# Optimization experiments

Measured on AMD Instinct MI355X. Metric: run time of the kernel, lower is better.

The kernel has to match this reference:

```python
import jax, jax.numpy as jnp
import numpy as np
import math

B, T, D, H, FFN_DIM, SE_HID = 16, 1024, 512, 8, 2048, 256
EPS = 1e-5  # torch LayerNorm default


def layer_norm(x, g, b):
    mu = jnp.mean(x, axis=-1, keepdims=True)
    var = jnp.mean((x - mu) ** 2, axis=-1, keepdims=True)
    return (x - mu) * jax.lax.rsqrt(var + EPS) * g + b


def setup_inputs() -> dict:
    key = jax.random.key(0)
    ks = jax.random.split(key, 8)
    s = 0.02
    return {
        "x": jax.random.normal(ks[0], (B, T, D), dtype=jnp.float32),
        "wq": jax.random.normal(ks[1], (D, D), dtype=jnp.float32) * s,
        "wk": jax.random.normal(ks[2], (D, D), dtype=jnp.float32) * s,
        "wv": jax.random.normal(ks[3], (D, D), dtype=jnp.float32) * s,
        "ln1_g": jnp.ones((D,), jnp.float32),
        "ln1_b": jnp.zeros((D,), jnp.float32),
        "se_w1": jax.random.normal(ks[4], (T, SE_HID), dtype=jnp.float32) * s,
        "se_w2": jax.random.normal(ks[5], (SE_HID, T), dtype=jnp.float32) * s,
        "ffn_g": jnp.ones((D,), jnp.float32),
        "ffn_b": jnp.zeros((D,), jnp.float32),
        "w1": jax.random.normal(ks[6], (D, FFN_DIM), dtype=jnp.float32) * s,
        "b1": jnp.zeros((FFN_DIM,), jnp.float32),
        "w2": jax.random.normal(ks[7], (FFN_DIM, D), dtype=jnp.float32) * s,
        "b2": jnp.zeros((D,), jnp.float32),
    }


def _forward(x, wq, wk, wv, ln1_g, ln1_b, se_w1, se_w2, ffn_g, ffn_b, w1, b1, w2, b2):
    # --- SE gate over the sequence axis: squeeze over feature dim D ---
    y = jnp.mean(x, axis=-1)                       # (B, T)
    gate = jax.nn.sigmoid(jax.nn.relu(y @ se_w1) @ se_w2)  # (B, T)
    x = x + x * gate[..., None]

    d = D // H
    n = layer_norm(x, ln1_g, ln1_b)
    q = (n @ wq).reshape(B, T, H, d)
    k = (n @ wk).reshape(B, T, H, d)
    v = (n @ wv).reshape(B, T, H, d)
    attn = jnp.einsum('bnhd,bmhd->bnmh', q, k) / math.sqrt(d)
    w = jax.nn.softmax(attn, axis=2)               # softmax over key dim m
    x = x + jnp.einsum('bnmh,bmhd->bnhd', w, v).reshape(B, T, D)

    # --- FFN (pre-norm, exact GELU as nn.GELU default) ---
    n2 = layer_norm(x, ffn_g, ffn_b)
    h = jax.nn.gelu(n2 @ w1 + b1, approximate=False)
    return x + (h @ w2 + b2)


def reference(x, wq, wk, wv, ln1_g, ln1_b, se_w1, se_w2, ffn_g, ffn_b, w1, b1, w2, b2):
    return _forward(x, wq, wk, wv, ln1_g, ln1_b, se_w1, se_w2, ffn_g, ffn_b, w1, b1, w2, b2)
```

## Files before the change

kernel.cpp:

```cpp
#include <hip/hip_runtime.h>

typedef unsigned int uint32;

using bf16x8 = __attribute__((ext_vector_type(8))) short;
using f32x4  = __attribute__((ext_vector_type(4))) float;

#define B_  16
#define T_  1024
#define D_  512
#define H_  8
#define HD_ 64
#define FFN_ 2048
#define SEH_ 256
#define EPS_ 1e-5f

#define AS1 __attribute__((address_space(1)))
#define AS3 __attribute__((address_space(3)))

__device__ __forceinline__ ushort f2bf(float f) {
  uint32 x = __float_as_uint(f);
  return (ushort)((x + 0x7fffu + ((x >> 16) & 1u)) >> 16);
}
__device__ __forceinline__ float bf2f(ushort u) {
  return __uint_as_float(((uint32)u) << 16);
}
__device__ __forceinline__ float gelu_fast(float v) {
  float u = v * (0.7978845608f + 0.0356774081f * v * v);
  float e = __expf(2.0f * u);
  float t = 1.0f - 2.0f * __builtin_amdgcn_rcpf(e + 1.0f);
  return 0.5f * v * (1.0f + t);
}

__global__ __launch_bounds__(256) void cast_transpose_all_k(
    const float* __restrict__ wq, const float* __restrict__ wk,
    const float* __restrict__ wv, const float* __restrict__ w1,
    const float* __restrict__ w2, ushort* __restrict__ wqkvT,
    ushort* __restrict__ w1T, ushort* __restrict__ w2T) {
  __shared__ float tile[32][33];
  int bid = blockIdx.x;
  const float* W; ushort* WT; int K, N, bk, bn;
  if (bid < 768) {
    int w = bid >> 8, r = bid & 255;
    W = (w == 0) ? wq : (w == 1) ? wk : wv;
    WT = wqkvT + (size_t)w * 512 * 512;
    K = 512; N = 512; bk = (r >> 4) * 32; bn = (r & 15) * 32;
  } else if (bid < 1792) {
    int r = bid - 768;
    W = w1; WT = w1T; K = 512; N = 2048; bk = (r >> 6) * 32; bn = (r & 63) * 32;
  } else {
    int r = bid - 1792;
    W = w2; WT = w2T; K = 2048; N = 512; bk = (r >> 4) * 32; bn = (r & 15) * 32;
  }
  int lx = threadIdx.x & 31;
  int ly = threadIdx.x >> 5;
  #pragma unroll
  for (int i = ly; i < 32; i += 8)
    tile[i][lx] = W[(size_t)(bk + i) * N + bn + lx];
  __syncthreads();
  #pragma unroll
  for (int i = ly; i < 32; i += 8)
    WT[(size_t)(bn + i) * K + bk + lx] = f2bf(tile[lx][i]);
}

__global__ __launch_bounds__(256) void se_rowmean_k(const float* __restrict__ x,
                                                    float* __restrict__ y) {
  int row  = blockIdx.x * 4 + (threadIdx.x >> 6);
  int lane = threadIdx.x & 63;
  const float4* p = (const float4*)(x + (size_t)row * D_);
  float4 a = p[lane * 2];
  float4 b = p[lane * 2 + 1];
  float s = a.x + a.y + a.z + a.w + b.x + b.y + b.z + b.w;
  #pragma unroll
  for (int m = 1; m < 64; m <<= 1) s += __shfl_xor(s, m);
  if (lane == 0) y[row] = s * (1.0f / D_);
}

__global__ __launch_bounds__(256) void se_mlp1_k(const float* __restrict__ y,
                                                 const float* __restrict__ w1,
                                                 float* __restrict__ z) {
  __shared__ float yb[T_];
  __shared__ float part[8][32];
  int b = blockIdx.x, jt = blockIdx.y;
  int tid = threadIdx.x;
  #pragma unroll
  for (int i = 0; i < 4; i++) yb[tid + i * 256] = y[(size_t)b * T_ + tid + i * 256];
  __syncthreads();
  int tj = tid & 31, tk = tid >> 5;
  int j = jt * 32 + tj;
  const float* wp = w1 + (size_t)(tk * 128) * SEH_ + j;
  const float* yp = yb + tk * 128;
  float a0 = 0.f, a1 = 0.f, a2 = 0.f, a3 = 0.f;
  #pragma unroll
  for (int t = 0; t < 128; t += 4) {
    a0 += yp[t]     * wp[(t)     * SEH_];
    a1 += yp[t + 1] * wp[(t + 1) * SEH_];
    a2 += yp[t + 2] * wp[(t + 2) * SEH_];
    a3 += yp[t + 3] * wp[(t + 3) * SEH_];
  }
  part[tk][tj] = (a0 + a1) + (a2 + a3);
  __syncthreads();
  if (tid < 32) {
    float s = 0.f;
    #pragma unroll
    for (int k = 0; k < 8; k++) s += part[k][tid];
    z[(size_t)b * SEH_ + jt * 32 + tid] = fmaxf(s, 0.f);
  }
}

__global__ __launch_bounds__(256) void se_mlp2_k(const float* __restrict__ z,
                                                 const float* __restrict__ w2,
                                                 float* __restrict__ gate) {
  __shared__ float zb[SEH_];
  __shared__ float part[2][128];
  int b = blockIdx.x, bt = blockIdx.y;
  int tid = threadIdx.x;
  zb[tid & 255] = z[(size_t)b * SEH_ + (tid & 255)];
  __syncthreads();
  int tt = tid & 127, tk = tid >> 7;
  int t = bt * 128 + tt;
  const float* wp = w2 + (size_t)(tk * 128) * T_ + t;
  const float* zp = zb + tk * 128;
  float a0 = 0.f, a1 = 0.f, a2 = 0.f, a3 = 0.f;
  #pragma unroll
  for (int j = 0; j < 128; j += 4) {
    a0 += zp[j]     * wp[(j)     * T_];
    a1 += zp[j + 1] * wp[(j + 1) * T_];
    a2 += zp[j + 2] * wp[(j + 2) * T_];
    a3 += zp[j + 3] * wp[(j + 3) * T_];
  }
  part[tk][tt] = (a0 + a1) + (a2 + a3);
  __syncthreads();
  if (tid < 128) {
    float s = part[0][tid] + part[1][tid];
    gate[(size_t)b * T_ + bt * 128 + tid] = 1.0f / (1.0f + __expf(-s));
  }
}

__global__ __launch_bounds__(256) void gate_ln1_k(
    const float* __restrict__ x, const float* __restrict__ gate,
    const float* __restrict__ g, const float* __restrict__ beta,
    float* __restrict__ x1, ushort* __restrict__ nbuf) {
  int rid  = blockIdx.x * 4 + (threadIdx.x >> 6);
  int lane = threadIdx.x & 63;
  const float4* xr = (const float4*)(x + (size_t)rid * D_);
  float4 a = xr[lane * 2];
  float4 b = xr[lane * 2 + 1];
  float gv = 1.0f + gate[rid];
  a.x *= gv; a.y *= gv; a.z *= gv; a.w *= gv;
  b.x *= gv; b.y *= gv; b.z *= gv; b.w *= gv;
  float4* x1r = (float4*)(x1 + (size_t)rid * D_);
  x1r[lane * 2]     = a;
  x1r[lane * 2 + 1] = b;
  float s  = a.x + a.y + a.z + a.w + b.x + b.y + b.z + b.w;
  float ss = a.x*a.x + a.y*a.y + a.z*a.z + a.w*a.w + b.x*b.x + b.y*b.y + b.z*b.z + b.w*b.w;
  #pragma unroll
  for (int m = 1; m < 64; m <<= 1) { s += __shfl_xor(s, m); ss += __shfl_xor(ss, m); }
  float mu   = s * (1.0f / D_);
  float var  = ss * (1.0f / D_) - mu * mu;
  float rstd = rsqrtf(var + EPS_);
  const float4* gp = (const float4*)g;
  const float4* bp = (const float4*)beta;
  float4 g0 = gp[lane * 2], g1 = gp[lane * 2 + 1];
  float4 b0 = bp[lane * 2], b1 = bp[lane * 2 + 1];
  union { uint4 v; ushort u[8]; } pk;
  pk.u[0] = f2bf((a.x - mu) * rstd * g0.x + b0.x);
  pk.u[1] = f2bf((a.y - mu) * rstd * g0.y + b0.y);
  pk.u[2] = f2bf((a.z - mu) * rstd * g0.z + b0.z);
  pk.u[3] = f2bf((a.w - mu) * rstd * g0.w + b0.w);
  pk.u[4] = f2bf((b.x - mu) * rstd * g1.x + b1.x);
  pk.u[5] = f2bf((b.y - mu) * rstd * g1.y + b1.y);
  pk.u[6] = f2bf((b.z - mu) * rstd * g1.z + b1.z);
  pk.u[7] = f2bf((b.w - mu) * rstd * g1.w + b1.w);
  *(uint4*)(nbuf + (size_t)rid * D_ + lane * 8) = pk.v;
}

__global__ __launch_bounds__(256) void ln2_k(
    const float* __restrict__ x2, const float* __restrict__ g,
    const float* __restrict__ beta, ushort* __restrict__ nbuf) {
  int rid  = blockIdx.x * 4 + (threadIdx.x >> 6);
  int lane = threadIdx.x & 63;
  const float4* xr = (const float4*)(x2 + (size_t)rid * D_);
  float4 a = xr[lane * 2];
  float4 b = xr[lane * 2 + 1];
  float s  = a.x + a.y + a.z + a.w + b.x + b.y + b.z + b.w;
  float ss = a.x*a.x + a.y*a.y + a.z*a.z + a.w*a.w + b.x*b.x + b.y*b.y + b.z*b.z + b.w*b.w;
  #pragma unroll
  for (int m = 1; m < 64; m <<= 1) { s += __shfl_xor(s, m); ss += __shfl_xor(ss, m); }
  float mu   = s * (1.0f / D_);
  float var  = ss * (1.0f / D_) - mu * mu;
  float rstd = rsqrtf(var + EPS_);
  const float4* gp = (const float4*)g;
  const float4* bp = (const float4*)beta;
  float4 g0 = gp[lane * 2], g1 = gp[lane * 2 + 1];
  float4 b0 = bp[lane * 2], b1 = bp[lane * 2 + 1];
  union { uint4 v; ushort u[8]; } pk;
  pk.u[0] = f2bf((a.x - mu) * rstd * g0.x + b0.x);
  pk.u[1] = f2bf((a.y - mu) * rstd * g0.y + b0.y);
  pk.u[2] = f2bf((a.z - mu) * rstd * g0.z + b0.z);
  pk.u[3] = f2bf((a.w - mu) * rstd * g0.w + b0.w);
  pk.u[4] = f2bf((b.x - mu) * rstd * g1.x + b1.x);
  pk.u[5] = f2bf((b.y - mu) * rstd * g1.y + b1.y);
  pk.u[6] = f2bf((b.z - mu) * rstd * g1.z + b1.z);
  pk.u[7] = f2bf((b.w - mu) * rstd * g1.w + b1.w);
  *(uint4*)(nbuf + (size_t)rid * D_ + lane * 8) = pk.v;
}

#define MFMA16 __builtin_amdgcn_mfma_f32_16x16x32_bf16
template <int BN>
__global__ __launch_bounds__(512, 2) void gemm256_k(
    const ushort* __restrict__ A, const ushort* __restrict__ BT,
    int M, int N, int K,
    const float* __restrict__ bias, const float* __restrict__ resid,
    ushort* __restrict__ outB, ushort* __restrict__ outB2,
    ushort* __restrict__ vTout, float* __restrict__ outF, int epi) {
  constexpr int WNS   = BN / 4;
  constexpr int NT    = BN / 64;
  constexpr int NH    = NT / 2;
  constexpr int BROWS = BN / 8;
  constexpr int BJ    = BN / 64;
  __shared__ ushort smem[2 * 256 * 64 + 2 * BN * 64];
  ushort* As = smem;
  ushort* Bs = smem + 2 * 256 * 64;

  int tid  = threadIdx.x;
  int wave = tid >> 6;
  int lane = tid & 63;
  int quad = lane >> 4;
  int l15  = lane & 15;
  int wm   = wave >> 2;
  int wn   = wave & 3;
  int lr   = lane >> 3;
  int lcs  = (lane & 7) ^ lr;

  int nbk = N / BN;
  int bid = blockIdx.x;
  int xcd = bid & 7;
  int sb  = bid >> 3;
  int n0  = (sb % nbk) * BN;
  int m0  = ((sb / nbk) * 8 + xcd) * 256;

  f32x4 acc[8][NT];
  #pragma unroll
  for (int i = 0; i < 8; i++)
    #pragma unroll
    for (int j = 0; j < NT; j++) acc[i][j] = (f32x4){0.f, 0.f, 0.f, 0.f};

  const ushort* Ag = A  + (size_t)(m0 + wave * 32 + lr) * K + lcs * 8;
  const ushort* Bg = BT + (size_t)(n0 + wave * BROWS + lr) * K + lcs * 8;

  auto STAGE = [&](int t, int buf) {
    int ko = t * 64;
    ushort* da = As + buf * (256 * 64) + wave * (32 * 64);
    #pragma unroll
    for (int j = 0; j < 4; j++)
      __builtin_amdgcn_global_load_lds((const AS1 void*)(Ag + ko + (size_t)(j * 8) * K),
                                       (AS3 void*)(da + j * 512), 16, 0, 0);
    ushort* db = Bs + buf * (BN * 64) + wave * (BROWS * 64);
    #pragma unroll
    for (int j = 0; j < BJ; j++)
      __builtin_amdgcn_global_load_lds((const AS1 void*)(Bg + ko + (size_t)(j * 8) * K),
                                       (AS3 void*)(db + j * 512), 16, 0, 0);
  };

  int ntt = K >> 6;
  STAGE(0, 0);
  STAGE(1, 1);
  if constexpr (BN == 256) asm volatile("s_waitcnt vmcnt(8)" ::: "memory");
  else                     asm volatile("s_waitcnt vmcnt(6)" ::: "memory");
  __builtin_amdgcn_s_barrier();

  const ushort* Arow = As + (wm * 128 + l15) * 64;
  const ushort* Brow = Bs + (wn * WNS + l15) * 64;
  int c0 = ((0 + quad) ^ (l15 & 7)) * 8;
  int c1 = ((4 + quad) ^ (l15 & 7)) * 8;

  for (int t = 0; t < ntt; ++t) {
    const ushort* Ab = Arow + (t & 1) * (256 * 64);
    const ushort* Bb = Brow + (t & 1) * (BN * 64);
    bf16x8 a[4][2], b[NT][2];

    #pragma unroll
    for (int m4 = 0; m4 < 4; m4++) {
      a[m4][0] = *(const bf16x8*)(Ab + m4 * 1024 + c0);
      a[m4][1] = *(const bf16x8*)(Ab + m4 * 1024 + c1);
    }
    #pragma unroll
    for (int h = 0; h < NH; h++) {
      b[h][0] = *(const bf16x8*)(Bb + h * 1024 + c0);
      b[h][1] = *(const bf16x8*)(Bb + h * 1024 + c1);
    }
    __builtin_amdgcn_s_barrier();
    asm volatile("s_waitcnt lgkmcnt(0)" ::: "memory");
    __builtin_amdgcn_sched_barrier(0);
    __builtin_amdgcn_s_setprio(1);
    #pragma unroll
    for (int m4 = 0; m4 < 4; m4++)
      #pragma unroll
      for (int h = 0; h < NH; h++) {
        acc[m4][h] = MFMA16(a[m4][0], b[h][0], acc[m4][h], 0, 0, 0);
        acc[m4][h] = MFMA16(a[m4][1], b[h][1], acc[m4][h], 0, 0, 0);
      }
    __builtin_amdgcn_s_setprio(0);
    __builtin_amdgcn_s_barrier();

    #pragma unroll
    for (int h = 0; h < NH; h++) {
      b[NH + h][0] = *(const bf16x8*)(Bb + (NH + h) * 1024 + c0);
      b[NH + h][1] = *(const bf16x8*)(Bb + (NH + h) * 1024 + c1);
    }
    __builtin_amdgcn_s_barrier();
    asm volatile("s_waitcnt lgkmcnt(0)" ::: "memory");
    __builtin_amdgcn_sched_barrier(0);
    __builtin_amdgcn_s_setprio(1);
    #pragma unroll
    for (int m4 = 0; m4 < 4; m4++)
      #pragma unroll
      for (int h = 0; h < NH; h++) {
        acc[m4][NH + h] = MFMA16(a[m4][0], b[NH + h][0], acc[m4][NH + h], 0, 0, 0);
        acc[m4][NH + h] = MFMA16(a[m4][1], b[NH + h][1], acc[m4][NH + h], 0, 0, 0);
      }
    __builtin_amdgcn_s_setprio(0);
    __builtin_amdgcn_s_barrier();

    #pragma unroll
    for (int m4 = 0; m4 < 4; m4++) {
      a[m4][0] = *(const bf16x8*)(Ab + (4 + m4) * 1024 + c0);
      a[m4][1] = *(const bf16x8*)(Ab + (4 + m4) * 1024 + c1);
    }
    __builtin_amdgcn_s_barrier();
    asm volatile("s_waitcnt lgkmcnt(0)" ::: "memory");
    __builtin_amdgcn_sched_barrier(0);
    __builtin_amdgcn_s_setprio(1);
    #pragma unroll
    for (int m4 = 0; m4 < 4; m4++)
      #pragma unroll
      for (int h = 0; h < NH; h++) {
        acc[4 + m4][h] = MFMA16(a[m4][0], b[h][0], acc[4 + m4][h], 0, 0, 0);
        acc[4 + m4][h] = MFMA16(a[m4][1], b[h][1], acc[4 + m4][h], 0, 0, 0);
      }
    __builtin_amdgcn_s_setprio(0);
    __builtin_amdgcn_s_barrier();

    __builtin_amdgcn_s_setprio(1);
    #pragma unroll
    for (int m4 = 0; m4 < 4; m4++)
      #pragma unroll
      for (int h = 0; h < NH; h++) {
        acc[4 + m4][NH + h] = MFMA16(a[m4][0], b[NH + h][0], acc[4 + m4][NH + h], 0, 0, 0);
        acc[4 + m4][NH + h] = MFMA16(a[m4][1], b[NH + h][1], acc[4 + m4][NH + h], 0, 0, 0);
      }
    __builtin_amdgcn_s_setprio(0);

    if (t + 1 < ntt) {
      if (t + 2 < ntt) {
        STAGE(t + 2, t & 1);
        if constexpr (BN == 256) asm volatile("s_waitcnt vmcnt(8)" ::: "memory");
        else                     asm volatile("s_waitcnt vmcnt(6)" ::: "memory");
      } else {
        asm volatile("s_waitcnt vmcnt(0)" ::: "memory");
      }
      __builtin_amdgcn_s_barrier();
    }
  }

  int colbase = n0 + wn * WNS;
  if (epi == 2) {
    #pragma unroll
    for (int nt = 0; nt < NT; nt++) {
      int n = colbase + nt * 16 + l15;
      float bv = bias[n];
      #pragma unroll
      for (int mt = 0; mt < 8; mt++) {
        int m = m0 + wm * 128 + mt * 16 + quad * 4;
        #pragma unroll
        for (int r = 0; r < 4; r++) {
          size_t idx = (size_t)(m + r) * N + n;
          outF[idx] = acc[mt][nt][r] + bv + resid[idx];
        }
      }
    }
  } else {
    __syncthreads();
    if (epi == 3 && n0 >= 1024) {
      constexpr int TST = 136;
      ushort* tb = smem + wave * (32 * TST);
      #pragma unroll
      for (int nt = 0; nt < NT; nt++) {
        int dloc = nt * 16 + l15;
        #pragma unroll
        for (int mt = 0; mt < 8; mt++) {
          ushort4 pk;
          pk.x = f2bf(acc[mt][nt][0]);
          pk.y = f2bf(acc[mt][nt][1]);
          pk.z = f2bf(acc[mt][nt][2]);
          pk.w = f2bf(acc[mt][nt][3]);
          *(ushort4*)(tb + dloc * TST + mt * 16 + quad * 4) = pk;
        }
      }
      int dbase = (n0 - 1024) + wn * WNS;
      int bb = m0 >> 10;
      int tg = (m0 & 1023) + wm * 128 + l15 * 8;
      #pragma unroll
      for (int j = 0; j < 8; j++) {
        int dloc = j * 4 + quad;
        int d = dbase + dloc;
        int hh = d >> 6, dd = d & 63;
        uint4 vv = *(const uint4*)(tb + dloc * TST + l15 * 8);
        *(uint4*)(vTout + (((size_t)bb * 8 + hh) * 64 + dd) * 1024 + tg) = vv;
      }
    } else {
      constexpr int RS  = WNS + 8;
      constexpr int LPR = WNS / 8;
      constexpr int RPS = 64 / LPR;
      ushort* tb = smem + wave * (32 * RS);
      ushort* gout; int ldN; float scl;
      if (epi == 1) { gout = outB; ldN = N; scl = 1.0f; }
      else {
        gout = (n0 < 512) ? outB : outB2; ldN = 512;
        scl = (n0 < 512) ? 0.18033688011112042f : 1.0f;
      }
      int ncol = (epi == 1) ? colbase : ((n0 & 511) + wn * WNS);
      float bv[NT];
      #pragma unroll
      for (int nt = 0; nt < NT; nt++)
        bv[nt] = (epi == 1) ? bias[colbase + nt * 16 + l15] : 0.0f;
      int rrow = lane / LPR;
      int seg  = lane % LPR;
      int mrow0 = m0 + wm * 128;
      #pragma unroll
      for (int mtg = 0; mtg < 4; mtg++) {
        #pragma unroll
        for (int mh = 0; mh < 2; mh++) {
          int mt = mtg * 2 + mh;
          #pragma unroll
          for (int nt = 0; nt < NT; nt++) {
            #pragma unroll
            for (int r = 0; r < 4; r++) {
              float v = (epi == 1) ? gelu_fast(acc[mt][nt][r] + bv[nt])
                                   : acc[mt][nt][r] * scl;
              tb[(mh * 16 + quad * 4 + r) * RS + nt * 16 + l15] = f2bf(v);
            }
          }
        }
        #pragma unroll
        for (int it = 0; it < 32 / RPS; it++) {
          int rl = it * RPS + rrow;
          uint4 v = *(const uint4*)(tb + rl * RS + seg * 8);
          *(uint4*)(gout + (size_t)(mrow0 + mtg * 32 + rl) * ldN + ncol + seg * 8) = v;
        }
      }
    }
  }
}

__global__ __launch_bounds__(256) void attn_k(
    const ushort* __restrict__ q, const ushort* __restrict__ k,
    const ushort* __restrict__ vT, const float* __restrict__ x1,
    float* __restrict__ out) {
  __shared__ ushort Ks[64 * 64];
  __shared__ ushort Vs[64 * 64];
  __shared__ ushort Ps[128 * 64];
  int bid = blockIdx.x;
  int xcd = bid & 7;
  int j   = bid >> 3;
  int qt  = j & 7;
  int pair = xcd * 16 + (j >> 3);
  int b = pair >> 3;
  int h = pair & 7;
  int t0 = qt * 128;
  int tid  = threadIdx.x;
  int wave = tid >> 6;
  int lane = tid & 63;
  int quad = lane >> 4;
  int l15  = lane & 15;

  const ushort* qp0 = q + ((size_t)(b * T_ + t0 + wave * 16 + l15)) * D_ + h * HD_;
  const ushort* qp1 = qp0 + (size_t)64 * D_;
  bf16x8 aq0 = *(const bf16x8*)(qp0 + quad * 8);
  bf16x8 aq1 = *(const bf16x8*)(qp0 + 32 + quad * 8);
  bf16x8 aq2 = *(const bf16x8*)(qp1 + quad * 8);
  bf16x8 aq3 = *(const bf16x8*)(qp1 + 32 + quad * 8);

  int srow = tid >> 2;
  int c2   = (tid & 3) * 2;
  int scol = c2 * 8;
  int sw0  = ((c2)     ^ (srow & 7)) << 3;
  int sw1  = ((c2 + 1) ^ (srow & 7)) << 3;
  int swb  = srow * 64;
  int rsw0 = ((quad)     ^ (l15 & 7)) << 3;
  int rsw1 = ((quad + 4) ^ (l15 & 7)) << 3;

  float l_part[2][4] = {{0.f, 0.f, 0.f, 0.f}, {0.f, 0.f, 0.f, 0.f}};
  f32x4 o0[4], o1[4];
  #pragma unroll
  for (int dt = 0; dt < 4; dt++) {
    o0[dt] = (f32x4){0.f, 0.f, 0.f, 0.f};
    o1[dt] = (f32x4){0.f, 0.f, 0.f, 0.f};
  }

  const ushort* vTb = vT + ((size_t)(b * 8 + h) * 64 + srow) * 1024 + scol;
  size_t kgb = ((size_t)(b * T_ + srow)) * D_ + h * HD_ + scol;

  uint4 ku0 = *(const uint4*)(k + kgb);
  uint4 ku1 = *(const uint4*)(k + kgb + 8);
  uint4 vv0 = *(const uint4*)(vTb);
  uint4 vv1 = *(const uint4*)(vTb + 8);

  for (int kt = 0; kt < 16; kt++) {
    __syncthreads();

    *(uint4*)(Ks + swb + sw0) = ku0;
    *(uint4*)(Ks + swb + sw1) = ku1;
    *(uint4*)(Vs + swb + sw0) = vv0;
    *(uint4*)(Vs + swb + sw1) = vv1;

    __syncthreads();

    if (kt + 1 < 16) {
      size_t kg2 = kgb + (size_t)(kt + 1) * 64 * D_;
      const ushort* vp2 = vTb + (kt + 1) * 64;
      ku0 = *(const uint4*)(k + kg2);
      ku1 = *(const uint4*)(k + kg2 + 8);
      vv0 = *(const uint4*)(vp2);
      vv1 = *(const uint4*)(vp2 + 8);
    }

    f32x4 s0[4], s1[4];
    #pragma unroll
    for (int nt = 0; nt < 4; nt++) {
      const ushort* krow = Ks + (nt * 16 + l15) * 64;
      bf16x8 bk0 = *(const bf16x8*)(krow + rsw0);
      bf16x8 bk1 = *(const bf16x8*)(krow + rsw1);
      f32x4 z = (f32x4){0.f, 0.f, 0.f, 0.f};
      s0[nt] = MFMA16(aq0, bk0, z, 0, 0, 0);
      s0[nt] = MFMA16(aq1, bk1, s0[nt], 0, 0, 0);
      s1[nt] = MFMA16(aq2, bk0, z, 0, 0, 0);
      s1[nt] = MFMA16(aq3, bk1, s1[nt], 0, 0, 0);
    }

    #pragma unroll
    for (int nt = 0; nt < 4; nt++) {
      int cps = nt * 2 + (l15 >> 3);
      #pragma unroll
      for (int r = 0; r < 4; r++) {
        int rowl = quad * 4 + r;
        int off = (wave * 16 + rowl) * 64 + ((cps ^ (rowl & 7)) << 3) + (l15 & 7);
        float p0 = __builtin_amdgcn_exp2f(s0[nt][r]);
        float p1 = __builtin_amdgcn_exp2f(s1[nt][r]);
        l_part[0][r] += p0;
        l_part[1][r] += p1;
        Ps[off]            = f2bf(p0);
        Ps[off + 64 * 64]  = f2bf(p1);
      }
    }

    const ushort* prow = Ps + (wave * 16 + l15) * 64;
    bf16x8 ap0 = *(const bf16x8*)(prow + rsw0);
    bf16x8 ap1 = *(const bf16x8*)(prow + rsw1);
    bf16x8 ap2 = *(const bf16x8*)(prow + 4096 + rsw0);
    bf16x8 ap3 = *(const bf16x8*)(prow + 4096 + rsw1);
    #pragma unroll
    for (int dt = 0; dt < 4; dt++) {
      const ushort* vrow = Vs + (dt * 16 + l15) * 64;
      bf16x8 bv0 = *(const bf16x8*)(vrow + rsw0);
      bf16x8 bv1 = *(const bf16x8*)(vrow + rsw1);
      o0[dt] = MFMA16(ap0, bv0, o0[dt], 0, 0, 0);
      o0[dt] = MFMA16(ap1, bv1, o0[dt], 0, 0, 0);
      o1[dt] = MFMA16(ap2, bv0, o1[dt], 0, 0, 0);
      o1[dt] = MFMA16(ap3, bv1, o1[dt], 0, 0, 0);
    }
  }

  #pragma unroll
  for (int s = 0; s < 2; s++) {
    f32x4* oo = s ? o1 : o0;
    #pragma unroll
    for (int r = 0; r < 4; r++) {
      float l = l_part[s][r];
      l += __shfl_xor(l, 1);
      l += __shfl_xor(l, 2);
      l += __shfl_xor(l, 4);
      l += __shfl_xor(l, 8);
      float inv = 1.0f / l;
      int qrow = t0 + s * 64 + wave * 16 + quad * 4 + r;
      size_t base = ((size_t)(b * T_ + qrow)) * D_ + h * HD_;
      #pragma unroll
      for (int dt = 0; dt < 4; dt++) {
        size_t idx = base + dt * 16 + l15;
        out[idx] = x1[idx] + oo[dt][r] * inv;
      }
    }
  }
}

extern "C" void kernel_launch(void* const* d_in, const int* in_sizes, int n_in,
                              void* d_out, int out_size, void* d_ws, size_t ws_size,
                              hipStream_t stream) {
  (void)in_sizes; (void)n_in; (void)out_size; (void)ws_size;
  const float* x     = (const float*)d_in[0];
  const float* wq    = (const float*)d_in[1];
  const float* wk    = (const float*)d_in[2];
  const float* wv    = (const float*)d_in[3];
  const float* ln1_g = (const float*)d_in[4];
  const float* ln1_b = (const float*)d_in[5];
  const float* se_w1 = (const float*)d_in[6];
  const float* se_w2 = (const float*)d_in[7];
  const float* ffn_g = (const float*)d_in[8];
  const float* ffn_b = (const float*)d_in[9];
  const float* w1    = (const float*)d_in[10];
  const float* b1    = (const float*)d_in[11];
  const float* w2    = (const float*)d_in[12];
  const float* b2    = (const float*)d_in[13];
  float* out = (float*)d_out;
  char* ws = (char*)d_ws;

  constexpr size_t X1_OFF   = 0;
  constexpr size_t N_OFF    = 33554432;
  constexpr size_t Q_OFF    = 50331648;
  constexpr size_t K_OFF    = 67108864;
  constexpr size_t V_OFF    = 83886080;
  constexpr size_t H_OFF    = 50331648;
  constexpr size_t WQKV_OFF = 117440512;
  constexpr size_t W1T_OFF  = 119013376;
  constexpr size_t W2T_OFF  = 121110528;
  constexpr size_t Y_OFF    = 123207680;
  constexpr size_t Z_OFF    = 123273216;
  constexpr size_t GATE_OFF = 123289600;

  float*  x1    = (float*)(ws + X1_OFF);
  ushort* nbuf  = (ushort*)(ws + N_OFF);
  ushort* qb    = (ushort*)(ws + Q_OFF);
  ushort* kb    = (ushort*)(ws + K_OFF);
  ushort* vT    = (ushort*)(ws + V_OFF);
  ushort* hb    = (ushort*)(ws + H_OFF);
  ushort* wqkvT = (ushort*)(ws + WQKV_OFF);
  ushort* w1T   = (ushort*)(ws + W1T_OFF);
  ushort* w2T   = (ushort*)(ws + W2T_OFF);
  float*  yv    = (float*)(ws + Y_OFF);
  float*  zv    = (float*)(ws + Z_OFF);
  float*  gate  = (float*)(ws + GATE_OFF);

  const int M = B_ * T_;

  cast_transpose_all_k<<<2816, 256, 0, stream>>>(wq, wk, wv, w1, w2, wqkvT, w1T, w2T);

  se_rowmean_k<<<M / 4, 256, 0, stream>>>(x, yv);
  se_mlp1_k<<<dim3(B_, 8), 256, 0, stream>>>(yv, se_w1, zv);
  se_mlp2_k<<<dim3(B_, 8), 256, 0, stream>>>(zv, se_w2, gate);

  gate_ln1_k<<<M / 4, 256, 0, stream>>>(x, gate, ln1_g, ln1_b, x1, nbuf);

  gemm256_k<128><<<(M / 256) * (1536 / 128), 512, 0, stream>>>(
      nbuf, wqkvT, M, 1536, D_, nullptr, nullptr, qb, kb, vT, nullptr, 3);

  attn_k<<<B_ * H_ * (T_ / 128), 256, 0, stream>>>(qb, kb, vT, x1, out);

  ln2_k<<<M / 4, 256, 0, stream>>>(out, ffn_g, ffn_b, nbuf);

  gemm256_k<256><<<(M / 256) * (FFN_ / 256), 512, 0, stream>>>(
      nbuf, w1T, M, FFN_, D_, b1, nullptr, hb, nullptr, nullptr, nullptr, 1);
  gemm256_k<128><<<(M / 256) * (D_ / 128), 512, 0, stream>>>(
      hb, w2T, M, D_, FFN_, b2, out, nullptr, nullptr, nullptr, out, 2);
}
```

Baseline: 344.7 us.

## Double-buffer attention K/V via direct global-to-LDS loads with larger query tiles

The attention kernel now handles 256 query rows per block with 512 threads, halving how often each K/V tile is loaded per query. K/V tiles are staged straight into double-buffered LDS with global_load_lds, so the register round trip is gone and the next tile's load overlaps compute. Each iteration needs one barrier instead of two. The softmax exp is fused into the QK loop and uses a packed bf16 convert. This uses more LDS per block and launches half as many blocks, which may lower occupancy and raise tail effects.

```diff
diff --git a/kernel.cpp b/kernel.cpp
--- a/kernel.cpp
+++ b/kernel.cpp
@@ -23,6 +23,11 @@
 }
 __device__ __forceinline__ float bf2f(ushort u) {
   return __uint_as_float(((uint32)u) << 16);
+}
+__device__ __forceinline__ uint32 cvtpk(float a, float b) {
+  uint32 r;
+  asm("v_cvt_pk_bf16_f32 %0, %1, %2" : "=v"(r) : "v"(a), "v"(b));
+  return r;
 }
 __device__ __forceinline__ float gelu_fast(float v) {
   float u = v * (0.7978845608f + 0.0356774081f * v * v);
@@ -453,40 +458,50 @@
   }
 }
 
-__global__ __launch_bounds__(256) void attn_k(
+__global__ __launch_bounds__(512, 2) void attn_k(
     const ushort* __restrict__ q, const ushort* __restrict__ k,
     const ushort* __restrict__ vT, const float* __restrict__ x1,
     float* __restrict__ out) {
-  __shared__ ushort Ks[64 * 64];
-  __shared__ ushort Vs[64 * 64];
-  __shared__ ushort Ps[128 * 64];
+  __shared__ ushort Ks[2 * 64 * 64];
+  __shared__ ushort Vs[2 * 64 * 64];
+  __shared__ ushort Ps[256 * 64];
   int bid = blockIdx.x;
   int xcd = bid & 7;
   int j   = bid >> 3;
-  int qt  = j & 7;
-  int pair = xcd * 16 + (j >> 3);
+  int qt  = j & 3;
+  int pair = xcd * 16 + (j >> 2);
   int b = pair >> 3;
   int h = pair & 7;
-  int t0 = qt * 128;
+  int t0 = qt * 256;
   int tid  = threadIdx.x;
   int wave = tid >> 6;
   int lane = tid & 63;
   int quad = lane >> 4;
   int l15  = lane & 15;
 
+  int row8 = lane >> 3;
+  int csw  = ((lane & 7) ^ row8) * 8;
+  const ushort* kst = k + ((size_t)(b * T_ + wave * 8 + row8)) * D_ + h * HD_ + csw;
+  const ushort* vst = vT + ((size_t)((b * 8 + h) * 64 + wave * 8 + row8)) * 1024 + csw;
+  ushort* KsW = Ks + wave * 512;
+  ushort* VsW = Vs + wave * 512;
+
+  auto STAGE = [&](int kt, int buf) {
+    __builtin_amdgcn_global_load_lds((const AS1 void*)(kst + (size_t)kt * 64 * D_),
+                                     (AS3 void*)(KsW + buf * 4096), 16, 0, 0);
+    __builtin_amdgcn_global_load_lds((const AS1 void*)(vst + kt * 64),
+                                     (AS3 void*)(VsW + buf * 4096), 16, 0, 0);
+  };
+
+  STAGE(0, 0);
+
   const ushort* qp0 = q + ((size_t)(b * T_ + t0 + wave * 16 + l15)) * D_ + h * HD_;
-  const ushort* qp1 = qp0 + (size_t)64 * D_;
+  const ushort* qp1 = qp0 + (size_t)128 * D_;
   bf16x8 aq0 = *(const bf16x8*)(qp0 + quad * 8);
   bf16x8 aq1 = *(const bf16x8*)(qp0 + 32 + quad * 8);
   bf16x8 aq2 = *(const bf16x8*)(qp1 + quad * 8);
   bf16x8 aq3 = *(const bf16x8*)(qp1 + 32 + quad * 8);
 
-  int srow = tid >> 2;
-  int c2   = (tid & 3) * 2;
-  int scol = c2 * 8;
-  int sw0  = ((c2)     ^ (srow & 7)) << 3;
-  int sw1  = ((c2 + 1) ^ (srow & 7)) << 3;
-  int swb  = srow * 64;
   int rsw0 = ((quad)     ^ (l15 & 7)) << 3;
   int rsw1 = ((quad + 4) ^ (l15 & 7)) << 3;
 
@@ -498,70 +513,58 @@
     o1[dt] = (f32x4){0.f, 0.f, 0.f, 0.f};
   }
 
-  const ushort* vTb = vT + ((size_t)(b * 8 + h) * 64 + srow) * 1024 + scol;
-  size_t kgb = ((size_t)(b * T_ + srow)) * D_ + h * HD_ + scol;
-
-  uint4 ku0 = *(const uint4*)(k + kgb);
-  uint4 ku1 = *(const uint4*)(k + kgb + 8);
-  uint4 vv0 = *(const uint4*)(vTb);
-  uint4 vv1 = *(const uint4*)(vTb + 8);
+  asm volatile("s_waitcnt vmcnt(0)" ::: "memory");
+  __syncthreads();
 
   for (int kt = 0; kt < 16; kt++) {
-    __syncthreads();
-
-    *(uint4*)(Ks + swb + sw0) = ku0;
-    *(uint4*)(Ks + swb + sw1) = ku1;
-    *(uint4*)(Vs + swb + sw0) = vv0;
-    *(uint4*)(Vs + swb + sw1) = vv1;
-
-    __syncthreads();
-
-    if (kt + 1 < 16) {
-      size_t kg2 = kgb + (size_t)(kt + 1) * 64 * D_;
-      const ushort* vp2 = vTb + (kt + 1) * 64;
-      ku0 = *(const uint4*)(k + kg2);
-      ku1 = *(const uint4*)(k + kg2 + 8);
-      vv0 = *(const uint4*)(vp2);
-      vv1 = *(const uint4*)(vp2 + 8);
-    }
-
-    f32x4 s0[4], s1[4];
+    int buf = kt & 1;
+    if (kt + 1 < 16) STAGE(kt + 1, buf ^ 1);
+    const ushort* Kb = Ks + buf * 4096;
+    const ushort* Vb = Vs + buf * 4096;
+
     #pragma unroll
     for (int nt = 0; nt < 4; nt++) {
-      const ushort* krow = Ks + (nt * 16 + l15) * 64;
+      const ushort* krow = Kb + (nt * 16 + l15) * 64;
       bf16x8 bk0 = *(const bf16x8*)(krow + rsw0);
       bf16x8 bk1 = *(const bf16x8*)(krow + rsw1);
       f32x4 z = (f32x4){0.f, 0.f, 0.f, 0.f};
-      s0[nt] = MFMA16(aq0, bk0, z, 0, 0, 0);
-      s0[nt] = MFMA16(aq1, bk1, s0[nt], 0, 0, 0);
-      s1[nt] = MFMA16(aq2, bk0, z, 0, 0, 0);
-      s1[nt] = MFMA16(aq3, bk1, s1[nt], 0, 0, 0);
-    }
-
-    #pragma unroll
-    for (int nt = 0; nt < 4; nt++) {
+      f32x4 s0 = MFMA16(aq0, bk0, z, 0, 0, 0);
+      s0 = MFMA16(aq1, bk1, s0, 0, 0, 0);
+      f32x4 s1 = MFMA16(aq2, bk0, z, 0, 0, 0);
+      s1 = MFMA16(aq3, bk1, s1, 0, 0, 0);
+
+      float p0[4], p1[4];
+      #pragma unroll
+      for (int r = 0; r < 4; r++) {
+        p0[r] = __builtin_amdgcn_exp2f(s0[r]);
+        p1[r] = __builtin_amdgcn_exp2f(s1[r]);
+        l_part[0][r] += p0[r];
+        l_part[1][r] += p1[r];
+      }
       int cps = nt * 2 + (l15 >> 3);
-      #pragma unroll
-      for (int r = 0; r < 4; r++) {
-        int rowl = quad * 4 + r;
-        int off = (wave * 16 + rowl) * 64 + ((cps ^ (rowl & 7)) << 3) + (l15 & 7);
-        float p0 = __builtin_amdgcn_exp2f(s0[nt][r]);
-        float p1 = __builtin_amdgcn_exp2f(s1[nt][r]);
-        l_part[0][r] += p0;
-        l_part[1][r] += p1;
-        Ps[off]            = f2bf(p0);
-        Ps[off + 64 * 64]  = f2bf(p1);
+      int cbase = l15 & 7;
+      #pragma unroll
+      for (int hs = 0; hs < 2; hs++) {
+        uint32 u01 = cvtpk(hs ? p1[0] : p0[0], hs ? p1[1] : p0[1]);
+        uint32 u23 = cvtpk(hs ? p1[2] : p0[2], hs ? p1[3] : p0[3]);
+        int rb = hs * 128 + wave * 16 + quad * 4;
+        #pragma unroll
+        for (int r = 0; r < 4; r++) {
+          int off = (rb + r) * 64 + ((cps ^ ((quad * 4 + r) & 7)) << 3) + cbase;
+          uint32 uu = (r < 2) ? u01 : u23;
+          Ps[off] = (ushort)((r & 1) ? (uu >> 16) : uu);
+        }
       }
     }
 
     const ushort* prow = Ps + (wave * 16 + l15) * 64;
     bf16x8 ap0 = *(const bf16x8*)(prow + rsw0);
     bf16x8 ap1 = *(const bf16x8*)(prow + rsw1);
-    bf16x8 ap2 = *(const bf16x8*)(prow + 4096 + rsw0);
-    bf16x8 ap3 = *(const bf16x8*)(prow + 4096 + rsw1);
+    bf16x8 ap2 = *(const bf16x8*)(prow + 8192 + rsw0);
+    bf16x8 ap3 = *(const bf16x8*)(prow + 8192 + rsw1);
     #pragma unroll
     for (int dt = 0; dt < 4; dt++) {
-      const ushort* vrow = Vs + (dt * 16 + l15) * 64;
+      const ushort* vrow = Vb + (dt * 16 + l15) * 64;
       bf16x8 bv0 = *(const bf16x8*)(vrow + rsw0);
       bf16x8 bv1 = *(const bf16x8*)(vrow + rsw1);
       o0[dt] = MFMA16(ap0, bv0, o0[dt], 0, 0, 0);
@@ -569,6 +572,8 @@
       o1[dt] = MFMA16(ap2, bv0, o1[dt], 0, 0, 0);
       o1[dt] = MFMA16(ap3, bv1, o1[dt], 0, 0, 0);
     }
+
+    __syncthreads();
   }
 
   #pragma unroll
@@ -582,7 +587,7 @@
       l += __shfl_xor(l, 4);
       l += __shfl_xor(l, 8);
       float inv = 1.0f / l;
-      int qrow = t0 + s * 64 + wave * 16 + quad * 4 + r;
+      int qrow = t0 + s * 128 + wave * 16 + quad * 4 + r;
       size_t base = ((size_t)(b * T_ + qrow)) * D_ + h * HD_;
       #pragma unroll
       for (int dt = 0; dt < 4; dt++) {
@@ -653,7 +658,7 @@
   gemm256_k<128><<<(M / 256) * (1536 / 128), 512, 0, stream>>>(
       nbuf, wqkvT, M, 1536, D_, nullptr, nullptr, qb, kb, vT, nullptr, 3);
 
-  attn_k<<<B_ * H_ * (T_ / 128), 256, 0, stream>>>(qb, kb, vT, x1, out);
+  attn_k<<<B_ * H_ * (T_ / 256), 512, 0, stream>>>(qb, kb, vT, x1, out);
 
   ln2_k<<<M / 4, 256, 0, stream>>>(out, ffn_g, ffn_b, nbuf);
 
```

New measurement: 331.7 us. 1.04x faster.
